# Kernel tuning notes

Measured on AMD Instinct MI355X. Metric: run time of the kernel, lower is better.

## Reference

```python
import jax, jax.numpy as jnp
import numpy as np

NEG_INF = -10000000.0


def setup_inputs() -> dict:
    key = jax.random.key(0)
    ks = jax.random.split(key, 9)
    B, S, H = 16, 2048, 1024
    std = 1.0 / np.sqrt(H)
    return {
        "queries": jax.random.normal(ks[0], (B, S, H), jnp.float32),
        "keys": jax.random.normal(ks[1], (B, S, H), jnp.float32),
        "values": jax.random.normal(ks[2], (B, S, H), jnp.float32),
        "Wq": jax.random.normal(ks[3], (H, H), jnp.float32) * std,
        "bq": jax.random.normal(ks[4], (H,), jnp.float32) * std,
        "Wk": jax.random.normal(ks[5], (H, H), jnp.float32) * std,
        "bk": jax.random.normal(ks[6], (H,), jnp.float32) * std,
        "Wv": jax.random.normal(ks[7], (H, H), jnp.float32) * std,
        "bv": jax.random.normal(ks[8], (H,), jnp.float32) * std,
    }


def reference(queries, keys, values, Wq, bq, Wk, bk, Wv, bv):
    H = queries.shape[-1]
    scale = jnp.asarray(1.0, queries.dtype) / jnp.sqrt(jnp.asarray(H, queries.dtype))
    # nn.Linear: x @ W.T + b
    q = queries @ Wq.T + bq          # [B, Q, H]
    k = keys @ Wk.T + bk             # [B, S, H]
    v = values @ Wv.T + bv           # [B, S, H]
    # torch: unnorm = k.bmm(q^T) -> [B, S, Q]; permuted to [B, Q, S] before softmax.
    scores = jnp.einsum('bqh,bsh->bqs', q, k) * scale   # [B, Q, S]
    Qlen, Slen = scores.shape[1], scores.shape[2]
    # tril(ones, diagonal=-1) on [S, Q]: entry (s, q) masked when s > q.
    # In the permuted [q, s] layout: mask where s > q (causal).
    mask = jnp.where(jnp.arange(Slen)[None, :] > jnp.arange(Qlen)[:, None],
                     jnp.asarray(NEG_INF, scores.dtype),
                     jnp.asarray(0.0, scores.dtype))
    attention_weights = jax.nn.softmax(scores + mask, axis=-1)  # [B, Q, S]
    context = jnp.einsum('bqs,bsh->bqh', attention_weights, v)  # [B, Q, H]
    # module returns attention_weights permuted back to [B, S, Q]
    return context, attention_weights.transpose(0, 2, 1)
```

## Files before the change

kernel.cpp:

```cpp
#include <hip/hip_runtime.h>
#include <hip/hip_bf16.h>
#include <cstdint>


typedef unsigned short u16;
typedef __bf16 bfrag __attribute__((ext_vector_type(8)));
typedef float f32x4 __attribute__((ext_vector_type(4)));

#define DEVI __device__ __forceinline__

DEVI u16 f2bf(float f) {
  unsigned u = __builtin_bit_cast(unsigned, f);
  u += 0x7FFFu + ((u >> 16) & 1u);
  return (u16)(u >> 16);
}

DEVI void g2l16(const void* g, void* l) {
  __builtin_amdgcn_global_load_lds(
      (const __attribute__((address_space(1))) void*)g,
      (__attribute__((address_space(3))) void*)l, 16, 0, 0);
}

__global__ void cast_f32_to_bf16(const float* __restrict__ in, u16* __restrict__ out, long n4) {
  long i = (long)blockIdx.x * blockDim.x + threadIdx.x;
  long stride = (long)gridDim.x * blockDim.x;
  for (long j = i; j < n4; j += stride) {
    float4 v = ((const float4*)in)[j];
    ushort4 o;
    o.x = f2bf(v.x); o.y = f2bf(v.y); o.z = f2bf(v.z); o.w = f2bf(v.w);
    ((ushort4*)out)[j] = o;
  }
}

template<int OUT_F32, int BIAS_MODE, int CAUSAL>
__global__ __launch_bounds__(512, 2)
void gemm_nt256(const u16* __restrict__ A, const u16* __restrict__ B,
                void* __restrict__ Cv, const float* __restrict__ bias,
                float scale, int K, long sA, long sB, long sC, int ldc,
                int gx, int gy)
{
  int nwg = gridDim.x * gridDim.y * gridDim.z;
  int hbid = blockIdx.x + gridDim.x * (blockIdx.y + gridDim.y * blockIdx.z);
  int cpx = nwg >> 3;
  int l = (hbid & 7) * cpx + (hbid >> 3);
  int bx = l % gx;
  int rest = l / gx;
  int by = rest % gy;
  int bz = rest / gy;

  long n0 = (long)bx * 256;
  long m0 = (long)by * 256;
  if (CAUSAL == 1 && m0 > n0 + 255) return;
  const u16* Ab = A + (long)bz * sA;
  const u16* Bb = B + (long)bz * sB;

  __shared__ __align__(16) u16 lA[2][256 * 64];
  __shared__ __align__(16) u16 lB[2][256 * 64];

  int tid = threadIdx.x;
  int lane = tid & 63;
  int wid = tid >> 6;
  int wr = wid >> 2;
  int wc = wid & 3;

  f32x4 acc[8][4] = {};

  int kmax = (CAUSAL == 2) ? ((K < m0 + 256) ? K : (int)(m0 + 256)) : K;
  int nkt = kmax >> 6;

  auto stage = [&](int kt, int bsel) {
    long k0 = (long)kt << 6;
    #pragma unroll
    for (int i = 0; i < 4; ++i) {
      int c = tid + (i << 9);
      int row = c >> 3;
      int sc = (c & 7) ^ (row & 7);
      g2l16(Ab + (m0 + row) * (long)K + k0 + (sc << 3), (char*)lA[bsel] + c * 16);
      g2l16(Bb + (n0 + row) * (long)K + k0 + (sc << 3), (char*)lB[bsel] + c * 16);
    }
  };

  stage(0, 0);
  __syncthreads();
  int cur = 0;
  for (int kt = 0; kt < nkt; ++kt) {
    if (kt + 1 < nkt) stage(kt + 1, cur ^ 1);
    const char* la = (const char*)lA[cur];
    const char* lb = (const char*)lB[cur];
    #pragma unroll
    for (int k2 = 0; k2 < 2; ++k2) {
      int kbc = (k2 << 2) + (lane >> 4);
      int rsel = lane & 15;
      bfrag af[8], bf[4];
      #pragma unroll
      for (int f = 0; f < 8; ++f) {
        int ra = wr * 128 + f * 16 + rsel;
        af[f] = *(const bfrag*)(la + ra * 128 + ((kbc ^ (ra & 7)) << 4));
      }
      #pragma unroll
      for (int f = 0; f < 4; ++f) {
        int rb = wc * 64 + f * 16 + rsel;
        bf[f] = *(const bfrag*)(lb + rb * 128 + ((kbc ^ (rb & 7)) << 4));
      }
      #pragma unroll
      for (int mi = 0; mi < 8; ++mi)
        #pragma unroll
        for (int ni = 0; ni < 4; ++ni)
          acc[mi][ni] = __builtin_amdgcn_mfma_f32_16x16x32_bf16(af[mi], bf[ni], acc[mi][ni], 0, 0, 0);
    }
    __syncthreads();
    cur ^= 1;
  }

  long cmb = m0 + wr * 128 + (lane >> 4) * 4;
  long cnb = n0 + wc * 64 + (lane & 15);
  #pragma unroll
  for (int mi = 0; mi < 8; ++mi) {
    #pragma unroll
    for (int ni = 0; ni < 4; ++ni) {
      f32x4 v = acc[mi][ni];
      long col = cnb + ni * 16;
      #pragma unroll
      for (int i = 0; i < 4; ++i) {
        long row = cmb + mi * 16 + i;
        float x = v[i] * scale;
        if (BIAS_MODE == 1) x += bias[col];
        if (BIAS_MODE == 2) x += bias[row];
        long cidx = (long)bz * sC + row * ldc + col;
        if (OUT_F32) ((float*)Cv)[cidx] = x;
        else         ((u16*)Cv)[cidx] = f2bf(x);
      }
    }
  }
}

__global__ __launch_bounds__(512)
void softmax_stats(const float* __restrict__ att, float* __restrict__ mo,
                   float* __restrict__ lo, int S) {
  int b  = blockIdx.y;
  int q0 = blockIdx.x * 64;
  int t  = threadIdx.x;
  int ql = t & 63;
  int grp = t >> 6;
  int q = q0 + ql;
  const float* a = att + (long)b * S * S + q;
  int send = q0 + 64;
  float m = -3.0e38f, l = 0.0f;
  for (int s = grp; s < send; s += 8) {
    float v = (s <= q) ? a[(long)s * S] : -3.0e38f;
    float mn = fmaxf(m, v);
    l = l * __expf(m - mn) + __expf(v - mn);
    m = mn;
  }
  __shared__ float sm[8][64], sl[8][64];
  sm[grp][ql] = m;
  sl[grp][ql] = l;
  __syncthreads();
  if (t < 64) {
    float M = sm[0][t];
    #pragma unroll
    for (int g = 1; g < 8; ++g) M = fmaxf(M, sm[g][t]);
    float L = 0.0f;
    #pragma unroll
    for (int g = 0; g < 8; ++g) L += sl[g][t] * __expf(sm[g][t] - M);
    mo[(long)b * S + q0 + t] = M;
    lo[(long)b * S + q0 + t] = L;
  }
}

__global__ void norm_transpose(float* __restrict__ att, const float* __restrict__ ms,
                               const float* __restrict__ ls, u16* __restrict__ probs, int S) {
  int b  = blockIdx.z;
  int q0 = blockIdx.x * 64;
  int s0 = blockIdx.y * 64;
  float* a = att + (long)b * S * S;
  u16* p = probs + (long)b * S * S;
  int tid = threadIdx.x;
  bool needp = s0 < ((q0 & ~255) + 256);

  if (s0 > q0 + 63) {
    float4 z = make_float4(0.f, 0.f, 0.f, 0.f);
    ushort4 zu; zu.x = zu.y = zu.z = zu.w = 0;
    #pragma unroll
    for (int it = 0; it < 4; ++it) {
      int j = tid + it * 256; int row = j >> 4; int c4 = (j & 15) * 4;
      *(float4*)&a[(long)(s0 + row) * S + q0 + c4] = z;
      if (needp) *(ushort4*)&p[(long)(q0 + row) * S + s0 + c4] = zu;
    }
    return;
  }

  __shared__ float t[64][65];
  __shared__ float lm[64], lr[64];
  if (tid < 64) {
    lm[tid] = ms[(long)b * S + q0 + tid];
    lr[tid] = 1.0f / ls[(long)b * S + q0 + tid];
  }
  __syncthreads();

  #pragma unroll
  for (int it = 0; it < 4; ++it) {
    int j = tid + it * 256; int row = j >> 4; int c4 = (j & 15) * 4;
    int s = s0 + row;
    float4 v = *(const float4*)&a[(long)s * S + q0 + c4];
    float vv[4] = {v.x, v.y, v.z, v.w};
    float oo[4];
    #pragma unroll
    for (int e = 0; e < 4; ++e) {
      int q = q0 + c4 + e;
      float pv = (s <= q) ? __expf(vv[e] - lm[c4 + e]) * lr[c4 + e] : 0.0f;
      oo[e] = pv;
      t[row][c4 + e] = pv;
    }
    float4 ov; ov.x = oo[0]; ov.y = oo[1]; ov.z = oo[2]; ov.w = oo[3];
    *(float4*)&a[(long)s * S + q0 + c4] = ov;
  }
  __syncthreads();

  #pragma unroll
  for (int it = 0; it < 4; ++it) {
    int j = tid + it * 256; int qrow = j >> 4; int sc4 = (j & 15) * 4;
    ushort4 ov;
    ov.x = f2bf(t[sc4 + 0][qrow]);
    ov.y = f2bf(t[sc4 + 1][qrow]);
    ov.z = f2bf(t[sc4 + 2][qrow]);
    ov.w = f2bf(t[sc4 + 3][qrow]);
    *(ushort4*)&p[(long)(q0 + qrow) * S + s0 + sc4] = ov;
  }
}

extern "C" void kernel_launch(void* const* d_in, const int* in_sizes, int n_in,
                              void* d_out, int out_size, void* d_ws, size_t ws_size,
                              hipStream_t stream) {
  const int B = 16, S = 2048, H = 1024;
  const long NE = (long)B * S * H;
  const float* Q  = (const float*)d_in[0];
  const float* Kk = (const float*)d_in[1];
  const float* V  = (const float*)d_in[2];
  const float* Wq = (const float*)d_in[3];
  const float* bq = (const float*)d_in[4];
  const float* Wk = (const float*)d_in[5];
  const float* bk = (const float*)d_in[6];
  const float* Wv = (const float*)d_in[7];
  const float* bv = (const float*)d_in[8];

  char* ws = (char*)d_ws;
  u16* xq    = (u16*)ws;
  u16* xk    = (u16*)(ws + (64L << 20));
  u16* xv    = (u16*)(ws + (128L << 20));
  u16* qb    = (u16*)(ws + (192L << 20));
  u16* kb    = (u16*)ws;
  u16* vT    = (u16*)(ws + (64L << 20));
  u16* probs = (u16*)(ws + (128L << 20));
  u16* Wqb   = (u16*)(ws + (256L << 20));
  u16* Wkb   = (u16*)(ws + (256L << 20) + (2L << 20));
  u16* Wvb   = (u16*)(ws + (256L << 20) + (4L << 20));
  float* mbuf = (float*)(ws + (256L << 20) + (6L << 20));
  float* lbuf = (float*)(ws + (256L << 20) + (6L << 20) + (1L << 17));

  float* ctx = (float*)d_out;
  float* att = (float*)d_out + NE;

  cast_f32_to_bf16<<<2048, 256, 0, stream>>>(Q,  xq, NE >> 2);
  cast_f32_to_bf16<<<2048, 256, 0, stream>>>(Kk, xk, NE >> 2);
  cast_f32_to_bf16<<<2048, 256, 0, stream>>>(V,  xv, NE >> 2);
  cast_f32_to_bf16<<<512, 256, 0, stream>>>(Wq, Wqb, ((long)H * H) >> 2);
  cast_f32_to_bf16<<<512, 256, 0, stream>>>(Wk, Wkb, ((long)H * H) >> 2);
  cast_f32_to_bf16<<<512, 256, 0, stream>>>(Wv, Wvb, ((long)H * H) >> 2);

  gemm_nt256<0, 1, 0><<<dim3(4, 128, 1), 512, 0, stream>>>(
      xq, Wqb, qb, bq, 1.0f, H, 0, 0, 0, H, 4, 128);
  gemm_nt256<0, 1, 0><<<dim3(4, 128, 1), 512, 0, stream>>>(
      xk, Wkb, kb, bk, 1.0f, H, 0, 0, 0, H, 4, 128);
  gemm_nt256<0, 2, 0><<<dim3(8, 4, 16), 512, 0, stream>>>(
      Wvb, xv, vT, bv, 1.0f, H, 0, (long)S * H, (long)H * S, S, 8, 4);

  gemm_nt256<1, 0, 1><<<dim3(8, 8, 16), 512, 0, stream>>>(
      kb, qb, att, nullptr, 0.03125f, H, (long)S * H, (long)S * H,
      (long)S * S, S, 8, 8);

  softmax_stats<<<dim3(32, 16), 512, 0, stream>>>(att, mbuf, lbuf, S);

  norm_transpose<<<dim3(32, 32, 16), 256, 0, stream>>>(att, mbuf, lbuf, probs, S);

  gemm_nt256<1, 0, 2><<<dim3(4, 8, 16), 512, 0, stream>>>(
      probs, vT, ctx, nullptr, 1.0f, S, (long)S * S, (long)H * S,
      (long)S * H, H, 4, 8);
}
```

Baseline: 815.1 us.

## Fuse cast kernels, relax GEMM occupancy bound, use nontemporal f32 stores

```diff
diff --git a/kernel.cpp b/kernel.cpp
--- a/kernel.cpp
+++ b/kernel.cpp
@@ -21,19 +21,33 @@
       (__attribute__((address_space(3))) void*)l, 16, 0, 0);
 }
 
-__global__ void cast_f32_to_bf16(const float* __restrict__ in, u16* __restrict__ out, long n4) {
+__global__ __launch_bounds__(256)
+void cast_all(const float* __restrict__ q, const float* __restrict__ k,
+              const float* __restrict__ v, const float* __restrict__ wq,
+              const float* __restrict__ wk, const float* __restrict__ wv,
+              u16* __restrict__ xq, u16* __restrict__ xk, u16* __restrict__ xv,
+              u16* __restrict__ owq, u16* __restrict__ owk, u16* __restrict__ owv,
+              long nbig4, long nsmall4) {
+  long total = 3 * nbig4 + 3 * nsmall4;
   long i = (long)blockIdx.x * blockDim.x + threadIdx.x;
   long stride = (long)gridDim.x * blockDim.x;
-  for (long j = i; j < n4; j += stride) {
-    float4 v = ((const float4*)in)[j];
+  for (long j = i; j < total; j += stride) {
+    const float4* src; ushort4* dst; long off;
+    if (j < nbig4)                { src = (const float4*)q;  dst = (ushort4*)xq;  off = j; }
+    else if (j < 2 * nbig4)       { src = (const float4*)k;  dst = (ushort4*)xk;  off = j - nbig4; }
+    else if (j < 3 * nbig4)       { src = (const float4*)v;  dst = (ushort4*)xv;  off = j - 2 * nbig4; }
+    else if (j < 3 * nbig4 + nsmall4)     { src = (const float4*)wq; dst = (ushort4*)owq; off = j - 3 * nbig4; }
+    else if (j < 3 * nbig4 + 2 * nsmall4) { src = (const float4*)wk; dst = (ushort4*)owk; off = j - 3 * nbig4 - nsmall4; }
+    else                          { src = (const float4*)wv; dst = (ushort4*)owv; off = j - 3 * nbig4 - 2 * nsmall4; }
+    float4 x = src[off];
     ushort4 o;
-    o.x = f2bf(v.x); o.y = f2bf(v.y); o.z = f2bf(v.z); o.w = f2bf(v.w);
-    ((ushort4*)out)[j] = o;
+    o.x = f2bf(x.x); o.y = f2bf(x.y); o.z = f2bf(x.z); o.w = f2bf(x.w);
+    dst[off] = o;
   }
 }
 
 template<int OUT_F32, int BIAS_MODE, int CAUSAL>
-__global__ __launch_bounds__(512, 2)
+__global__ __launch_bounds__(512, 1)
 void gemm_nt256(const u16* __restrict__ A, const u16* __restrict__ B,
                 void* __restrict__ Cv, const float* __restrict__ bias,
                 float scale, int K, long sA, long sB, long sC, int ldc,
@@ -81,10 +95,10 @@
   };
 
   stage(0, 0);
-  __syncthreads();
   int cur = 0;
-  for (int kt = 0; kt < nkt; ++kt) {
-    if (kt + 1 < nkt) stage(kt + 1, cur ^ 1);
+  for (int t = 0; t < nkt; ++t) {
+    if (t == 0) __syncthreads();
+    if (t + 1 < nkt) stage(t + 1, cur ^ 1);
     const char* la = (const char*)lA[cur];
     const char* lb = (const char*)lB[cur];
     #pragma unroll
@@ -127,8 +141,11 @@
         if (BIAS_MODE == 1) x += bias[col];
         if (BIAS_MODE == 2) x += bias[row];
         long cidx = (long)bz * sC + row * ldc + col;
-        if (OUT_F32) ((float*)Cv)[cidx] = x;
-        else         ((u16*)Cv)[cidx] = f2bf(x);
+        if (OUT_F32) {
+          __builtin_nontemporal_store(x, (float*)Cv + cidx);
+        } else {
+          ((u16*)Cv)[cidx] = f2bf(x);
+        }
       }
     }
   }
@@ -261,12 +278,9 @@
   float* ctx = (float*)d_out;
   float* att = (float*)d_out + NE;
 
-  cast_f32_to_bf16<<<2048, 256, 0, stream>>>(Q,  xq, NE >> 2);
-  cast_f32_to_bf16<<<2048, 256, 0, stream>>>(Kk, xk, NE >> 2);
-  cast_f32_to_bf16<<<2048, 256, 0, stream>>>(V,  xv, NE >> 2);
-  cast_f32_to_bf16<<<512, 256, 0, stream>>>(Wq, Wqb, ((long)H * H) >> 2);
-  cast_f32_to_bf16<<<512, 256, 0, stream>>>(Wk, Wkb, ((long)H * H) >> 2);
-  cast_f32_to_bf16<<<512, 256, 0, stream>>>(Wv, Wvb, ((long)H * H) >> 2);
+  cast_all<<<4096, 256, 0, stream>>>(Q, Kk, V, Wq, Wk, Wv,
+                                     xq, xk, xv, Wqb, Wkb, Wvb,
+                                     NE >> 2, ((long)H * H) >> 2);
 
   gemm_nt256<0, 1, 0><<<dim3(4, 128, 1), 512, 0, stream>>>(
       xq, Wqb, qb, bq, 1.0f, H, 0, 0, 0, H, 4, 128);
```

New measurement: 908.5 us. 11.5% more time.
